# Optimization experiments

Measured on AMD Instinct MI355X. Metric: run time of the kernel, lower is better.

## Reference

```python
import jax, jax.numpy as jnp
import numpy as np

B, K, S, L, D, A = 16, 128, 64, 2, 256, 500  # batch, beam, stack, layers, hidden, max_actions


def setup_inputs() -> dict:
    key = jax.random.key(0)
    k = jax.random.split(key, 8)
    return {
        "gen_ll": jax.random.normal(k[0], (B, K), jnp.float32),
        "trees": jax.random.normal(k[1], (B, K, S, D), jnp.float32),
        "hiddens": jax.random.normal(k[2], (B, K, S + 1, L, D), jnp.float32),
        "cells": jax.random.normal(k[3], (B, K, S + 1, L, D), jnp.float32),
        "actions": jax.random.randint(k[4], (B, K, A), 0, 100, dtype=jnp.int64)
        if jax.config.jax_enable_x64 else jax.random.randint(k[4], (B, K, A), 0, 100),
        "actions_pos": jax.random.randint(k[5], (B, K), 0, A - 1),
        "pointer": jax.random.randint(k[6], (B, K), 0, S),
        "beam_widths": jax.random.randint(k[7], (B,), 1, K + 1),  # >= 1 active beam per batch
    }


def _gather_beam(x, sort_idx):
    # gather along beam dim (axis=1) with broadcast over trailing dims
    idx = sort_idx.reshape(sort_idx.shape + (1,) * (x.ndim - 2))
    return jnp.take_along_axis(x, idx, axis=1)


def reference(gen_ll, trees, hiddens, cells, actions, actions_pos, pointer, beam_widths):
    # BeamItems.shrink(): mask beams outside active width, sort by score desc,
    # then reorder every parallel tensor (stack + action path) by sort_idx.
    order = jnp.arange(K)
    active = order[None, :] < beam_widths[:, None]                    # [B, K] active_idx_mask
    gen_ll_m = jnp.where(active, gen_ll, -jnp.inf)
    sort_idx = jnp.argsort(-gen_ll_m, axis=1)                          # descending sort
    gen_ll_s = jnp.take_along_axis(gen_ll_m, sort_idx, axis=1)

    trees_s = _gather_beam(trees, sort_idx)                            # stack.sort_by
    hiddens_s = _gather_beam(hiddens, sort_idx)
    cells_s = _gather_beam(cells, sort_idx)
    actions_s = _gather_beam(actions, sort_idx)                        # action_path.sort_by
    actions_pos_s = jnp.take_along_axis(actions_pos, sort_idx, axis=1)
    pointer_s = jnp.take_along_axis(pointer, sort_idx, axis=1)         # stack_state.sort_by

    new_beam_widths = jnp.minimum(beam_widths, K)
    # BeamItems.marginal_probs(): logsumexp over active beams (inactive already -inf)
    marginal = jax.nn.logsumexp(gen_ll_s, axis=1)                      # [B]
    # ActionPath.prev_actions(): gather at actions_pos
    prev_actions = jnp.take_along_axis(actions_s, actions_pos_s[:, :, None], axis=2)[:, :, 0]

    return (gen_ll_s, trees_s, hiddens_s, cells_s, marginal,
            actions_s, actions_pos_s, pointer_s, prev_actions, new_beam_widths)
```

## Files before the change

### kernel.cpp

```cpp
#include <hip/hip_runtime.h>
#include <math.h>

#define B 16
#define K 128
#define S 64
#define L 2
#define D 256
#define A 500

#define ROW4_TREES 4096
#define HALF4_HID  4160

#define NEG_BIG (-1.0e30f)

typedef float f32x4 __attribute__((ext_vector_type(4)));
typedef int   i32x4 __attribute__((ext_vector_type(4)));

#define OFF_GENLL 0
#define OFF_TREES 2048
#define OFF_HID   33556480
#define OFF_CELLS 101713920
#define OFF_MARG  169871360
#define OFF_ACT   169871376
#define OFF_APOS  170895376
#define OFF_PTR   170897424
#define OFF_PREV  170899472
#define OFF_NBW   170901520

#define NBLK 2048
#define NU_TREES 2048
#define UPB 5

template<int N4>
__device__ __forceinline__ void copy_unit(const f32x4* __restrict__ s,
                                          f32x4* __restrict__ d, int tid)
{
    constexpr int FULL = N4 / 256;
    constexpr int REM  = N4 % 256;
    for (int g = 0; g < FULL; g += 8) {
        f32x4 v[8];
#pragma unroll
        for (int i = 0; i < 8; ++i)
            v[i] = __builtin_nontemporal_load(&s[(g + i) * 256 + tid]);
#pragma unroll
        for (int i = 0; i < 8; ++i)
            __builtin_nontemporal_store(v[i], &d[(g + i) * 256 + tid]);
    }
    if (REM && tid < REM) {
        f32x4 v = __builtin_nontemporal_load(&s[FULL * 256 + tid]);
        __builtin_nontemporal_store(v, &d[FULL * 256 + tid]);
    }
}

__global__ void __launch_bounds__(128)
k_sort(const float* __restrict__ gen_ll,
       const int* __restrict__ actions,
       const int* __restrict__ actions_pos,
       const int* __restrict__ pointer,
       const int* __restrict__ beam_widths,
       float* __restrict__ out,
       int* __restrict__ sort_idx)
{
    const int b = blockIdx.x;
    const int k = threadIdx.x;

    __shared__ float key[K];
    __shared__ int   sidx[K];
    __shared__ float red[4];

    const int w = beam_widths[b];
    const float my = (k < w) ? gen_ll[b * K + k] : NEG_BIG;
    key[k] = my;
    __syncthreads();

    int rank = 0;
#pragma unroll 16
    for (int i = 0; i < K; ++i) {
        const float ki = key[i];
        rank += (ki > my) || (ki == my && i < k);
    }
    sidx[rank] = k;
    __syncthreads();

    const int j = sidx[k];
    sort_idx[b * K + k] = j;

    out[OFF_GENLL + b * K + k] = key[j];
    const int ap = actions_pos[b * K + j];
    out[OFF_APOS + b * K + k] = (float)ap;
    out[OFF_PTR  + b * K + k] = (float)pointer[b * K + j];
    out[OFF_PREV + b * K + k] = (float)actions[(size_t)(b * K + j) * A + ap];

    float m = my;
#pragma unroll
    for (int mask = 32; mask >= 1; mask >>= 1)
        m = fmaxf(m, __shfl_xor(m, mask, 64));
    if ((k & 63) == 0) red[k >> 6] = m;
    __syncthreads();
    m = fmaxf(red[0], red[1]);
    float e = expf(my - m);
#pragma unroll
    for (int mask = 32; mask >= 1; mask >>= 1)
        e += __shfl_xor(e, mask, 64);
    if ((k & 63) == 0) red[2 + (k >> 6)] = e;
    __syncthreads();
    if (k == 0) {
        out[OFF_MARG + b] = m + logf(red[2] + red[3]);
        out[OFF_NBW + b] = (float)(w < K ? w : K);
    }
}

__global__ void __launch_bounds__(256, 8)
k_copy(const f32x4* __restrict__ trees,
       const f32x4* __restrict__ hiddens,
       const f32x4* __restrict__ cells,
       const int* __restrict__ actions,
       const int* __restrict__ sort_idx,
       float* __restrict__ out)
{
    const int tid = threadIdx.x;
    const int bid = blockIdx.x;

    const int u0 = bid * UPB;
#pragma unroll
    for (int q = 0; q < UPB; ++q) {
        const int u = u0 + q;
        if (u < NU_TREES) {
            const int b = u >> 7, k = u & 127;
            const int j = sort_idx[(b << 7) + k];
            copy_unit<ROW4_TREES>(trees + (size_t)(b * K + j) * ROW4_TREES,
                                  (f32x4*)(out + OFF_TREES) + (size_t)u * ROW4_TREES,
                                  tid);
        } else {
            const int u2 = u - NU_TREES;
            const int which = u2 >> 12;
            const int u3 = u2 & 4095;
            const int row = u3 >> 1, half = u3 & 1;
            const int b = row >> 7, k = row & 127;
            const int j = sort_idx[(b << 7) + k];
            const f32x4* src = (which ? cells : hiddens)
                             + ((size_t)(b * K + j) * 2 + half) * HALF4_HID;
            f32x4* dst = (f32x4*)(out + (which ? OFF_CELLS : OFF_HID))
                       + (size_t)u3 * HALF4_HID;
            copy_unit<HALF4_HID>(src, dst, tid);
        }
    }

    {
        const int b = bid >> 7;
        const int j = sort_idx[bid];
        const i32x4* s = (const i32x4*)actions + (size_t)(b * K + j) * 125;
        f32x4* d = (f32x4*)(out + OFF_ACT) + (size_t)bid * 125;
        if (tid < 125) {
            const i32x4 v = __builtin_nontemporal_load(&s[tid]);
            f32x4 f;
            f.x = (float)v.x; f.y = (float)v.y; f.z = (float)v.z; f.w = (float)v.w;
            __builtin_nontemporal_store(f, &d[tid]);
        }
    }
}

extern "C" void kernel_launch(void* const* d_in, const int* in_sizes, int n_in,
                              void* d_out, int out_size, void* d_ws, size_t ws_size,
                              hipStream_t stream)
{
    const float* gen_ll      = (const float*)d_in[0];
    const float* trees       = (const float*)d_in[1];
    const float* hiddens     = (const float*)d_in[2];
    const float* cells       = (const float*)d_in[3];
    const int*   actions     = (const int*)d_in[4];
    const int*   actions_pos = (const int*)d_in[5];
    const int*   pointer     = (const int*)d_in[6];
    const int*   beam_widths = (const int*)d_in[7];
    float* out = (float*)d_out;
    int* sort_idx = (int*)d_ws;

    k_sort<<<B, K, 0, stream>>>(gen_ll, actions, actions_pos, pointer,
                                beam_widths, out, sort_idx);
    k_copy<<<NBLK, 256, 0, stream>>>((const f32x4*)trees, (const f32x4*)hiddens,
                                     (const f32x4*)cells, actions, sort_idx, out);
}
```

Measured before the change: 272.3 us.

## Replace per-row block copies with grid-stride flat region copies per tensor

The copy kernel stops assigning whole rows to blocks and instead splits the grid into fixed groups of blocks for trees, hiddens, cells and actions. Each group grid-strides over the flattened output, looking up the source row through a precomputed global source-row table. Each thread keeps four loads in flight per iteration, down from eight, and the hidden and cell paths need an integer division per element. The goal is to balance bandwidth across blocks and avoid tail imbalance, at the cost of extra index arithmetic and less memory-level parallelism per thread.

```diff
diff --git a/kernel.cpp b/kernel.cpp
--- a/kernel.cpp
+++ b/kernel.cpp
@@ -7,9 +7,6 @@
 #define L 2
 #define D 256
 #define A 500
-
-#define ROW4_TREES 4096
-#define HALF4_HID  4160
 
 #define NEG_BIG (-1.0e30f)
 
@@ -27,30 +24,18 @@
 #define OFF_PREV  170899472
 #define OFF_NBW   170901520
 
-#define NBLK 2048
-#define NU_TREES 2048
-#define UPB 5
+#define ROW4_T 4096
+#define ROW4_H 8320
+#define AROW4  125
+#define N4_T   (2048 * ROW4_T)
+#define N4_H   (2048 * ROW4_H)
+#define N4_A   (2048 * AROW4)
 
-template<int N4>
-__device__ __forceinline__ void copy_unit(const f32x4* __restrict__ s,
-                                          f32x4* __restrict__ d, int tid)
-{
-    constexpr int FULL = N4 / 256;
-    constexpr int REM  = N4 % 256;
-    for (int g = 0; g < FULL; g += 8) {
-        f32x4 v[8];
-#pragma unroll
-        for (int i = 0; i < 8; ++i)
-            v[i] = __builtin_nontemporal_load(&s[(g + i) * 256 + tid]);
-#pragma unroll
-        for (int i = 0; i < 8; ++i)
-            __builtin_nontemporal_store(v[i], &d[(g + i) * 256 + tid]);
-    }
-    if (REM && tid < REM) {
-        f32x4 v = __builtin_nontemporal_load(&s[FULL * 256 + tid]);
-        __builtin_nontemporal_store(v, &d[FULL * 256 + tid]);
-    }
-}
+#define NB_T 398
+#define NB_H 809
+#define NB_C 809
+#define NB_A 32
+#define NBLK (NB_T + NB_H + NB_C + NB_A)
 
 __global__ void __launch_bounds__(128)
 k_sort(const float* __restrict__ gen_ll,
@@ -59,7 +44,7 @@
        const int* __restrict__ pointer,
        const int* __restrict__ beam_widths,
        float* __restrict__ out,
-       int* __restrict__ sort_idx)
+       int* __restrict__ srcrow)
 {
     const int b = blockIdx.x;
     const int k = threadIdx.x;
@@ -83,7 +68,7 @@
     __syncthreads();
 
     const int j = sidx[k];
-    sort_idx[b * K + k] = j;
+    srcrow[b * K + k] = b * K + j;
 
     out[OFF_GENLL + b * K + k] = key[j];
     const int ap = actions_pos[b * K + j];
@@ -110,52 +95,75 @@
     }
 }
 
+template<int ROW4, bool POW2>
+__device__ __forceinline__ void region_copy(const f32x4* __restrict__ src,
+                                            f32x4* __restrict__ dst,
+                                            const int* __restrict__ srcrow,
+                                            int start, int stride, int n4)
+{
+    int i = start;
+    for (; i + 3 * stride < n4; i += 4 * stride) {
+        const int i0 = i, i1 = i + stride, i2 = i + 2 * stride, i3 = i + 3 * stride;
+        int r0, r1, r2, r3, o0, o1, o2, o3;
+        if (POW2) {
+            r0 = i0 >> 12; o0 = i0 & (ROW4 - 1);
+            r1 = i1 >> 12; o1 = i1 & (ROW4 - 1);
+            r2 = i2 >> 12; o2 = i2 & (ROW4 - 1);
+            r3 = i3 >> 12; o3 = i3 & (ROW4 - 1);
+        } else {
+            r0 = i0 / ROW4; o0 = i0 - r0 * ROW4;
+            r1 = i1 / ROW4; o1 = i1 - r1 * ROW4;
+            r2 = i2 / ROW4; o2 = i2 - r2 * ROW4;
+            r3 = i3 / ROW4; o3 = i3 - r3 * ROW4;
+        }
+        const f32x4 v0 = __builtin_nontemporal_load(&src[(size_t)srcrow[r0] * ROW4 + o0]);
+        const f32x4 v1 = __builtin_nontemporal_load(&src[(size_t)srcrow[r1] * ROW4 + o1]);
+        const f32x4 v2 = __builtin_nontemporal_load(&src[(size_t)srcrow[r2] * ROW4 + o2]);
+        const f32x4 v3 = __builtin_nontemporal_load(&src[(size_t)srcrow[r3] * ROW4 + o3]);
+        __builtin_nontemporal_store(v0, &dst[i0]);
+        __builtin_nontemporal_store(v1, &dst[i1]);
+        __builtin_nontemporal_store(v2, &dst[i2]);
+        __builtin_nontemporal_store(v3, &dst[i3]);
+    }
+    for (; i < n4; i += stride) {
+        const int r = POW2 ? (i >> 12) : (i / ROW4);
+        const int o = POW2 ? (i & (ROW4 - 1)) : (i - r * ROW4);
+        const f32x4 v = __builtin_nontemporal_load(&src[(size_t)srcrow[r] * ROW4 + o]);
+        __builtin_nontemporal_store(v, &dst[i]);
+    }
+}
+
 __global__ void __launch_bounds__(256, 8)
 k_copy(const f32x4* __restrict__ trees,
        const f32x4* __restrict__ hiddens,
        const f32x4* __restrict__ cells,
-       const int* __restrict__ actions,
-       const int* __restrict__ sort_idx,
+       const i32x4* __restrict__ actions,
+       const int* __restrict__ srcrow,
        float* __restrict__ out)
 {
     const int tid = threadIdx.x;
     const int bid = blockIdx.x;
 
-    const int u0 = bid * UPB;
-#pragma unroll
-    for (int q = 0; q < UPB; ++q) {
-        const int u = u0 + q;
-        if (u < NU_TREES) {
-            const int b = u >> 7, k = u & 127;
-            const int j = sort_idx[(b << 7) + k];
-            copy_unit<ROW4_TREES>(trees + (size_t)(b * K + j) * ROW4_TREES,
-                                  (f32x4*)(out + OFF_TREES) + (size_t)u * ROW4_TREES,
-                                  tid);
-        } else {
-            const int u2 = u - NU_TREES;
-            const int which = u2 >> 12;
-            const int u3 = u2 & 4095;
-            const int row = u3 >> 1, half = u3 & 1;
-            const int b = row >> 7, k = row & 127;
-            const int j = sort_idx[(b << 7) + k];
-            const f32x4* src = (which ? cells : hiddens)
-                             + ((size_t)(b * K + j) * 2 + half) * HALF4_HID;
-            f32x4* dst = (f32x4*)(out + (which ? OFF_CELLS : OFF_HID))
-                       + (size_t)u3 * HALF4_HID;
-            copy_unit<HALF4_HID>(src, dst, tid);
-        }
-    }
-
-    {
-        const int b = bid >> 7;
-        const int j = sort_idx[bid];
-        const i32x4* s = (const i32x4*)actions + (size_t)(b * K + j) * 125;
-        f32x4* d = (f32x4*)(out + OFF_ACT) + (size_t)bid * 125;
-        if (tid < 125) {
-            const i32x4 v = __builtin_nontemporal_load(&s[tid]);
+    if (bid < NB_T) {
+        region_copy<ROW4_T, true>(trees, (f32x4*)(out + OFF_TREES), srcrow,
+                                  bid * 256 + tid, NB_T * 256, N4_T);
+    } else if (bid < NB_T + NB_H) {
+        region_copy<ROW4_H, false>(hiddens, (f32x4*)(out + OFF_HID), srcrow,
+                                   (bid - NB_T) * 256 + tid, NB_H * 256, N4_H);
+    } else if (bid < NB_T + NB_H + NB_C) {
+        region_copy<ROW4_H, false>(cells, (f32x4*)(out + OFF_CELLS), srcrow,
+                                   (bid - NB_T - NB_H) * 256 + tid, NB_C * 256, N4_H);
+    } else {
+        f32x4* dst = (f32x4*)(out + OFF_ACT);
+        const int start = (bid - NB_T - NB_H - NB_C) * 256 + tid;
+        const int stride = NB_A * 256;
+        for (int i = start; i < N4_A; i += stride) {
+            const int r = i / AROW4;
+            const int o = i - r * AROW4;
+            const i32x4 v = __builtin_nontemporal_load(&actions[(size_t)srcrow[r] * AROW4 + o]);
             f32x4 f;
             f.x = (float)v.x; f.y = (float)v.y; f.z = (float)v.z; f.w = (float)v.w;
-            __builtin_nontemporal_store(f, &d[tid]);
+            __builtin_nontemporal_store(f, &dst[i]);
         }
     }
 }
@@ -173,10 +181,11 @@
     const int*   pointer     = (const int*)d_in[6];
     const int*   beam_widths = (const int*)d_in[7];
     float* out = (float*)d_out;
-    int* sort_idx = (int*)d_ws;
+    int* srcrow = (int*)d_ws;
 
     k_sort<<<B, K, 0, stream>>>(gen_ll, actions, actions_pos, pointer,
-                                beam_widths, out, sort_idx);
+                                beam_widths, out, srcrow);
     k_copy<<<NBLK, 256, 0, stream>>>((const f32x4*)trees, (const f32x4*)hiddens,
-                                     (const f32x4*)cells, actions, sort_idx, out);
+                                     (const f32x4*)cells, (const i32x4*)actions,
+                                     srcrow, out);
 }
```

New measurement: 268.4 us. About the same (-1.5%).
